# Performance work log

Measured on AMD Instinct MI355X. Metric: run time of the kernel, lower is better.

The kernel has to match this reference:

```python
import jax, jax.numpy as jnp
import numpy as np

RADIUS = 3
T_STEPS = 2
NEG = -9.0e8
B, L, DEG = 256, 64, 6
FEAT, BOND, FP, OUT = 39, 10, 256, 1


def _leaky(x):
    return jax.nn.leaky_relu(x, 0.01)


def _gru(x, h, wih, whh, bih, bhh):
    # PyTorch GRUCell: gates ordered (r, z, n)
    gi = x @ wih.T + bih
    gh = h @ whh.T + bhh
    ir, iz, inn = jnp.split(gi, 3, axis=-1)
    hr, hz, hn = jnp.split(gh, 3, axis=-1)
    r = jax.nn.sigmoid(ir + hr)
    z = jax.nn.sigmoid(iz + hz)
    n = jnp.tanh(inn + r * hn)
    return (1.0 - z) * n + z * h


def _forward(atom_list, bond_list, atom_mask,
             atom_fc_w, atom_fc_b, neighbor_fc_w, neighbor_fc_b,
             align_w, align_b, attend_w, attend_b,
             gru_wih, gru_whh, gru_bih, gru_bhh,
             mol_align_w, mol_align_b, mol_attend_w, mol_attend_b,
             mol_gru_wih, mol_gru_whh, mol_gru_bih, mol_gru_bhh,
             out_w, out_b,
             atom_degree_list, bond_degree_list):
    b, l, _ = atom_list.shape
    mask = atom_mask[..., None]                                   # [B,L,1]
    atom_feature = _leaky(atom_list @ atom_fc_w.T + atom_fc_b)    # [B,L,FP]

    # per-molecule neighbor gather (padding index = L-1)
    bidx = jnp.arange(b)[:, None, None]
    atom_nb = atom_list[bidx, atom_degree_list]                    # [B,L,deg,FEAT]
    bond_nb = bond_list[bidx, bond_degree_list]                    # [B,L,deg,BOND]
    neighbor_feature = _leaky(
        jnp.concatenate([atom_nb, bond_nb], axis=-1) @ neighbor_fc_w.T + neighbor_fc_b
    )                                                              # [B,L,deg,FP]

    attend_mask = (atom_degree_list != l - 1).astype(atom_feature.dtype)[..., None]
    softmax_mask = jnp.where(atom_degree_list == l - 1, NEG, 0.0).astype(atom_feature.dtype)[..., None]

    for d in range(RADIUS):
        af_exp = jnp.broadcast_to(atom_feature[:, :, None, :], neighbor_feature.shape)
        feature_align = jnp.concatenate([af_exp, neighbor_feature], axis=-1)  # [B,L,deg,2FP]
        align_score = _leaky(feature_align @ align_w[d].T + align_b[d]) + softmax_mask
        attention_weight = jax.nn.softmax(align_score, axis=-2) * attend_mask
        attended = neighbor_feature @ attend_w[d].T + attend_b[d]
        context = jax.nn.elu(jnp.sum(attention_weight * attended, axis=-2))   # [B,L,FP]
        atom_feature = _gru(context.reshape(b * l, -1), atom_feature.reshape(b * l, -1),
                            gru_wih[d], gru_whh[d], gru_bih[d], gru_bhh[d]).reshape(b, l, -1)
        # faithful to original: self-feature broadcast across neighbor dim
        neighbor_feature = jnp.broadcast_to(jax.nn.relu(atom_feature)[:, :, None, :],
                                            neighbor_feature.shape)

    mol_feature = jnp.sum(jax.nn.relu(atom_feature) * mask, axis=-2)          # [B,FP]
    mol_softmax_mask = jnp.where(atom_mask == 0, NEG, 0.0).astype(atom_feature.dtype)[..., None]

    for _ in range(T_STEPS):
        m_exp = jnp.broadcast_to(mol_feature[:, None, :], atom_feature.shape)
        mol_align = jnp.concatenate([m_exp, atom_feature], axis=-1)           # [B,L,2FP]
        mol_score = _leaky(mol_align @ mol_align_w.T + mol_align_b) + mol_softmax_mask
        mol_w = jax.nn.softmax(mol_score, axis=-2) * mask
        attended = atom_feature @ mol_attend_w.T + mol_attend_b
        mol_context = jax.nn.elu(jnp.sum(mol_w * attended, axis=-2))
        mol_feature = _gru(mol_context, mol_feature,
                           mol_gru_wih, mol_gru_whh, mol_gru_bih, mol_gru_bhh)

    mol_prediction = mol_feature @ out_w.T + out_b
    return atom_feature, mol_prediction


def setup_inputs() -> dict:
    key = jax.random.key(0)
    ks = jax.random.split(key, 20)
    s = 0.05
    return {
        "atom_list": jax.random.normal(ks[0], (B, L, FEAT), jnp.float32),
        "bond_list": jax.random.normal(ks[1], (B, L, BOND), jnp.float32),
        "atom_degree_list": jax.random.randint(ks[2], (B, L, DEG), 0, L),
        "bond_degree_list": jax.random.randint(ks[3], (B, L, DEG), 0, L),
        "atom_mask": jnp.ones((B, L), jnp.float32),
        "atom_fc_w": jax.random.normal(ks[4], (FP, FEAT)) * s,
        "atom_fc_b": jnp.zeros((FP,)),
        "neighbor_fc_w": jax.random.normal(ks[5], (FP, FEAT + BOND)) * s,
        "neighbor_fc_b": jnp.zeros((FP,)),
        "align_w": jax.random.normal(ks[6], (RADIUS, 1, 2 * FP)) * s,
        "align_b": jnp.zeros((RADIUS, 1)),
        "attend_w": jax.random.normal(ks[7], (RADIUS, FP, FP)) * s,
        "attend_b": jnp.zeros((RADIUS, FP)),
        "gru_wih": jax.random.normal(ks[8], (RADIUS, 3 * FP, FP)) * s,
        "gru_whh": jax.random.normal(ks[9], (RADIUS, 3 * FP, FP)) * s,
        "gru_bih": jnp.zeros((RADIUS, 3 * FP)),
        "gru_bhh": jnp.zeros((RADIUS, 3 * FP)),
        "mol_align_w": jax.random.normal(ks[10], (1, 2 * FP)) * s,
        "mol_align_b": jnp.zeros((1,)),
        "mol_attend_w": jax.random.normal(ks[11], (FP, FP)) * s,
        "mol_attend_b": jnp.zeros((FP,)),
        "mol_gru_wih": jax.random.normal(ks[12], (3 * FP, FP)) * s,
        "mol_gru_whh": jax.random.normal(ks[13], (3 * FP, FP)) * s,
        "mol_gru_bih": jnp.zeros((3 * FP,)),
        "mol_gru_bhh": jnp.zeros((3 * FP,)),
        "out_w": jax.random.normal(ks[14], (OUT, FP)) * s,
        "out_b": jnp.zeros((OUT,)),
    }


def reference(atom_list, bond_list, atom_degree_list, bond_degree_list, atom_mask,
              atom_fc_w, atom_fc_b, neighbor_fc_w, neighbor_fc_b,
              align_w, align_b, attend_w, attend_b,
              gru_wih, gru_whh, gru_bih, gru_bhh,
              mol_align_w, mol_align_b, mol_attend_w, mol_attend_b,
              mol_gru_wih, mol_gru_whh, mol_gru_bih, mol_gru_bhh,
              out_w, out_b):
    return _forward(atom_list, bond_list, atom_mask,
                    atom_fc_w, atom_fc_b, neighbor_fc_w, neighbor_fc_b,
                    align_w, align_b, attend_w, attend_b,
                    gru_wih, gru_whh, gru_bih, gru_bhh,
                    mol_align_w, mol_align_b, mol_attend_w, mol_attend_b,
                    mol_gru_wih, mol_gru_whh, mol_gru_bih, mol_gru_bhh,
                    out_w, out_b,
                    atom_degree_list, bond_degree_list)
```

## Files before the change

kernel.cpp:

```cpp
#include <hip/hip_runtime.h>
#include <hip/hip_bf16.h>

#define NB 256
#define NL 64
#define DEG 6
#define FEAT 39
#define BOND 10
#define FP 256
#define NEGV (-9.0e8f)

using s16x8 = __attribute__((ext_vector_type(8))) short;
using f32x4 = __attribute__((ext_vector_type(4))) float;

__device__ __forceinline__ unsigned short f2bf(float f){
  unsigned u = __float_as_uint(f);
  u += 0x7fffu + ((u >> 16) & 1u);
  return (unsigned short)(u >> 16);
}
__device__ __forceinline__ float lo16(unsigned u){ return __uint_as_float(u << 16); }
__device__ __forceinline__ float hi16(unsigned u){ return __uint_as_float(u & 0xffff0000u); }

__device__ __forceinline__ float block_sum256(float v, float* scr){
  #pragma unroll
  for(int o=32;o>0;o>>=1) v += __shfl_down(v, o, 64);
  __syncthreads();
  if((threadIdx.x & 63) == 0) scr[threadIdx.x >> 6] = v;
  __syncthreads();
  return scr[0] + scr[1] + scr[2] + scr[3];
}
__device__ __forceinline__ float wave_allsum(float v){
  #pragma unroll
  for(int o=1;o<64;o<<=1) v += __shfl_xor(v, o, 64);
  return v;
}

#define MCVT_N0 65536
#define MCVT_N1 196608
#define MCVT_N2 196608
#define MCVT_TOT (MCVT_N0+MCVT_N1+MCVT_N2)
#define CTXPK_N (3*8*8192)
#define GPK_N   (3*2*8*24576)
#define HALF_U16 24576

__global__ void k_cvt_mol(const float* __restrict__ a0, const float* __restrict__ a1,
                          const float* __restrict__ a2, unsigned short* __restrict__ dst){
  int i = blockIdx.x*256 + threadIdx.x;
  if(i >= MCVT_TOT) return;
  int off = i; const float* src;
  if(off < MCVT_N0) src = a0;
  else { off -= MCVT_N0;
    if(off < MCVT_N1) src = a1;
    else { off -= MCVT_N1; src = a2; } }
  dst[i] = f2bf(src[off]);
}

__global__ void k_pack(const float* __restrict__ attend_w, const float* __restrict__ gru_wih,
                       const float* __restrict__ gru_whh,
                       unsigned short* __restrict__ ctx_pk, unsigned short* __restrict__ gates_pk){
  int i = blockIdx.x*256 + threadIdx.x;
  if(i < CTXPK_N){
    int d = i >> 16;
    int rem = i & 65535;
    int kk = rem >> 13;
    int r2 = rem & 8191;
    int g = r2 >> 9;
    int l = (r2 >> 3) & 63;
    int q = r2 & 7;
    int row = g*16 + (l & 15);
    int k = kk*32 + (l >> 4)*8 + q;
    ctx_pk[i] = f2bf(attend_w[((size_t)d*256 + row)*256 + k]);
  } else {
    int j = i - CTXPK_N;
    if(j >= GPK_N) return;
    int d = j / 393216;
    int rem = j - d*393216;
    int nc = rem / 196608; rem -= nc*196608;
    int kk = rem / 24576;  rem -= kk*24576;
    int f = rem >> 9;
    int l = (rem >> 3) & 63;
    int q = rem & 7;
    int s = f >> 3, g = f & 7;
    int row = nc*128 + g*16 + (l & 15);
    int k = kk*32 + (l >> 4)*8 + q;
    float v = (s < 3) ? gru_wih[(((size_t)d*3 + s)*256 + row)*256 + k]
                      : gru_whh[(((size_t)d*3 + (s-3))*256 + row)*256 + k];
    gates_pk[j] = f2bf(v);
  }
}

__global__ void k_tr(const float* __restrict__ aw, const float* __restrict__ nw,
                     float* __restrict__ afcT, unsigned short* __restrict__ nfcT){
  int i = blockIdx.x*256 + threadIdx.x;
  if(i < 40*256){
    int k = i >> 8, r = i & 255;
    afcT[i] = (k < FEAT) ? aw[r*FEAT + k] : 0.f;
  } else {
    int j = i - 40*256;
    int k = j >> 8, r = j & 255;
    nfcT[j] = (k < FEAT+BOND) ? f2bf(nw[r*(FEAT+BOND) + k]) : (unsigned short)0;
  }
}

__global__ __launch_bounds__(256) void k_atom4(const float* __restrict__ atom,
    const float* __restrict__ afcT, const float* __restrict__ bias, float* __restrict__ af){
  __shared__ float x_s[4][40];
  const int t = threadIdx.x, bl0 = blockIdx.x*4;
  for(int idx=t; idx<4*FEAT; idx+=256){ int a=idx/FEAT, k=idx%FEAT; x_s[a][k]=atom[(bl0+a)*FEAT+k]; }
  if(t < 4) x_s[t][39] = 0.f;
  __syncthreads();
  const int w = t>>6, t0 = (t&63)*4, row = bl0 + w;
  float4 b4 = *(const float4*)&bias[t0];
  float acc[4] = {b4.x, b4.y, b4.z, b4.w};
  for(int k=0;k<40;++k){
    float iv = x_s[w][k];
    float4 wv = *(const float4*)&afcT[(k<<8)+t0];
    acc[0]=fmaf(iv,wv.x,acc[0]); acc[1]=fmaf(iv,wv.y,acc[1]);
    acc[2]=fmaf(iv,wv.z,acc[2]); acc[3]=fmaf(iv,wv.w,acc[3]);
  }
  float4 o;
  o.x = acc[0]>0.f?acc[0]:0.01f*acc[0]; o.y = acc[1]>0.f?acc[1]:0.01f*acc[1];
  o.z = acc[2]>0.f?acc[2]:0.01f*acc[2]; o.w = acc[3]>0.f?acc[3]:0.01f*acc[3];
  *(float4*)&af[(size_t)row*FP + t0] = o;
}

__global__ __launch_bounds__(256) void k_nbr4(const float* __restrict__ atom,
    const float* __restrict__ bond, const int* __restrict__ adl, const int* __restrict__ bdl,
    const unsigned short* __restrict__ nfcT, const float* __restrict__ bn,
    const float* __restrict__ alw, const float* __restrict__ alb,
    const float* __restrict__ af, float* __restrict__ wnf, float* __restrict__ swb){
  __shared__ float in_s[4][DEG][52];
  __shared__ int   ai_s[4][DEG];
  const int t = threadIdx.x, bl0 = blockIdx.x*4;
  if(t < 24){ int a=t/6, d=t%6; ai_s[a][d] = adl[(bl0+a)*DEG + d]; }
  __syncthreads();
  for(int idx=t; idx<4*DEG*(FEAT+BOND); idx+=256){
    int a = idx/(DEG*(FEAT+BOND)), rem = idx%(DEG*(FEAT+BOND));
    int d = rem/(FEAT+BOND), k = rem%(FEAT+BOND);
    int bb = (bl0+a) >> 6;
    float v;
    if(k < FEAT) v = atom[((size_t)bb*NL + ai_s[a][d])*FEAT + k];
    else { int bi = bdl[(bl0+a)*DEG + d]; v = bond[((size_t)bb*NL + bi)*BOND + (k-FEAT)]; }
    in_s[a][d][k] = v;
  }
  if(t < 24){ int a=t/6, d=t%6; in_s[a][d][49]=0.f; in_s[a][d][50]=0.f; in_s[a][d][51]=0.f; }
  __syncthreads();
  const int w = t>>6, lane = t&63, t0 = lane*4, row = bl0 + w;
  float acc[DEG][4] = {};
  for(int k=0;k<52;++k){
    uint2 u = *(const uint2*)&nfcT[(k<<8) + t0];
    float w0=lo16(u.x), w1=hi16(u.x), w2=lo16(u.y), w3=hi16(u.y);
    #pragma unroll
    for(int d=0;d<DEG;++d){
      float iv = in_s[w][d][k];
      acc[d][0]=fmaf(iv,w0,acc[d][0]); acc[d][1]=fmaf(iv,w1,acc[d][1]);
      acc[d][2]=fmaf(iv,w2,acc[d][2]); acc[d][3]=fmaf(iv,w3,acc[d][3]);
    }
  }
  float4 bnv = *(const float4*)&bn[t0];
  float bna[4] = {bnv.x, bnv.y, bnv.z, bnv.w};
  float nf[DEG][4];
  #pragma unroll
  for(int d=0;d<DEG;++d)
    #pragma unroll
    for(int j=0;j<4;++j){ float v = acc[d][j] + bna[j]; nf[d][j] = v>0.f ? v : 0.01f*v; }
  float4 af4 = *(const float4*)&af[(size_t)row*FP + t0];
  float4 a1  = *(const float4*)&alw[t0];
  float4 a2  = *(const float4*)&alw[FP + t0];
  float sa = wave_allsum(af4.x*a1.x + af4.y*a1.y + af4.z*a1.z + af4.w*a1.w);
  float sd[DEG];
  #pragma unroll
  for(int d=0;d<DEG;++d)
    sd[d] = wave_allsum(nf[d][0]*a2.x + nf[d][1]*a2.y + nf[d][2]*a2.z + nf[d][3]*a2.w);
  float ab = alb[0];
  float sc[DEG], msk[DEG];
  #pragma unroll
  for(int d=0;d<DEG;++d){
    float v = sa + sd[d] + ab;
    v = v>0.f ? v : 0.01f*v;
    msk[d] = (ai_s[w][d] == NL-1) ? 0.f : 1.f;
    sc[d] = v + (msk[d] > 0.f ? 0.f : NEGV);
  }
  float m = sc[0];
  #pragma unroll
  for(int d=1;d<DEG;++d) m = fmaxf(m, sc[d]);
  float e[DEG], Z = 0.f;
  #pragma unroll
  for(int d=0;d<DEG;++d){ e[d] = expf(sc[d]-m); Z += e[d]; }
  float wgt[DEG], sw = 0.f;
  #pragma unroll
  for(int d=0;d<DEG;++d){ wgt[d] = e[d]/Z*msk[d]; sw += wgt[d]; }
  float o[4] = {};
  #pragma unroll
  for(int d=0;d<DEG;++d)
    #pragma unroll
    for(int j=0;j<4;++j) o[j] = fmaf(wgt[d], nf[d][j], o[j]);
  float4 ov; ov.x=o[0]; ov.y=o[1]; ov.z=o[2]; ov.w=o[3];
  *(float4*)&wnf[(size_t)row*FP + t0] = ov;
  if(lane == 0) swb[row] = sw;
}

__global__ __launch_bounds__(512) void k_radius2(
    const float* __restrict__ wnf, float* __restrict__ af, const float* __restrict__ swb,
    const unsigned short* __restrict__ ctx_pk, const unsigned short* __restrict__ gates_pk,
    const float* __restrict__ attend_b,
    const float* __restrict__ gru_bih, const float* __restrict__ gru_bhh){
  __shared__ __align__(16) unsigned short Cf[32*512];
  __shared__ __align__(16) unsigned short Bu[2][HALF_U16];
  const int t = threadIdx.x;
  const int w = t>>6, lane = t&63, lr = lane&15, ks = lane>>4;
  const int wm = w>>2, wn = w&3;
  const int m0 = blockIdx.x*64;

  s16x8 pf[6]; int pfn = 0;
  auto LOADS = [&](int s){
    if(s >= 72) return;
    int d2 = s/24, r = s - d2*24;
    const unsigned short* src; int n;
    if(r < 8){ n = 2; src = ctx_pk + ((size_t)d2*8 + r)*8192; }
    else { int g = r - 8; n = 6; src = gates_pk + ((size_t)(d2*2 + (g>>3))*8 + (g&7))*24576; }
    pfn = n;
    #pragma unroll
    for(int c=0;c<6;++c) if(c < n) pf[c] = *(const s16x8*)(src + (w + c*8)*512 + lane*8);
  };
  auto WRITET = [&](int h){
    #pragma unroll
    for(int c=0;c<6;++c) if(c < pfn) *(s16x8*)&Bu[h][(w + c*8)*512 + lane*8] = pf[c];
  };

  LOADS(0);
  WRITET(0);
  LOADS(1);
  int half = 0;

  for(int d=0; d<3; ++d){
    const float* bat  = attend_b + d*256;
    const float* bihd = gru_bih + d*768;
    const float* bhhd = gru_bhh + d*768;

    __syncthreads();
    float4 px0[2], px1[2];
    #pragma unroll
    for(int mf=0; mf<2; ++mf){
      int row = m0 + wm*32 + mf*16 + lr;
      const float* sp = (d==0 ? wnf : af) + (size_t)row*256 + ks*8;
      px0[mf] = *(const float4*)sp; px1[mf] = *(const float4*)(sp+4);
    }
    f32x4 acc2[2][4] = {};
    for(int kk=0; kk<8; ++kk){
      int s = d*24 + kk;
      __syncthreads();
      WRITET(half^1);
      LOADS(s+2);
      float4 cx0[2] = {px0[0], px0[1]};
      float4 cx1[2] = {px1[0], px1[1]};
      if(kk < 7){
        #pragma unroll
        for(int mf=0; mf<2; ++mf){
          int row = m0 + wm*32 + mf*16 + lr;
          const float* sp = (d==0 ? wnf : af) + (size_t)row*256 + (kk+1)*32 + ks*8;
          px0[mf] = *(const float4*)sp; px1[mf] = *(const float4*)(sp+4);
        }
      }
      s16x8 xf[2];
      #pragma unroll
      for(int mf=0; mf<2; ++mf){
        float4 v0 = cx0[mf], v1 = cx1[mf];
        if(d != 0){
          float sw = swb[m0 + wm*32 + mf*16 + lr];
          v0.x=fmaxf(v0.x,0.f)*sw; v0.y=fmaxf(v0.y,0.f)*sw;
          v0.z=fmaxf(v0.z,0.f)*sw; v0.w=fmaxf(v0.w,0.f)*sw;
          v1.x=fmaxf(v1.x,0.f)*sw; v1.y=fmaxf(v1.y,0.f)*sw;
          v1.z=fmaxf(v1.z,0.f)*sw; v1.w=fmaxf(v1.w,0.f)*sw;
        }
        unsigned short tmp[8] = {f2bf(v0.x),f2bf(v0.y),f2bf(v0.z),f2bf(v0.w),
                                 f2bf(v1.x),f2bf(v1.y),f2bf(v1.z),f2bf(v1.w)};
        xf[mf] = *(s16x8*)tmp;
      }
      #pragma unroll
      for(int nf=0; nf<4; ++nf){
        s16x8 wf = *(const s16x8*)&Bu[half][((wn*4 + nf)*64 + lane)*8];
        acc2[0][nf] = __builtin_amdgcn_mfma_f32_16x16x32_bf16(wf, xf[0], acc2[0][nf],0,0,0);
        acc2[1][nf] = __builtin_amdgcn_mfma_f32_16x16x32_bf16(wf, xf[1], acc2[1][nf],0,0,0);
      }
      half ^= 1;
    }
    #pragma unroll
    for(int mf=0; mf<2; ++mf){
      float swv = swb[m0 + wm*32 + mf*16 + lr];
      #pragma unroll
      for(int nf=0; nf<4; ++nf){
        int nb = wn*64 + nf*16 + ks*4;
        float4 b4 = *(const float4*)&bat[nb];
        float bj[4] = {b4.x, b4.y, b4.z, b4.w};
        unsigned short o4[4];
        #pragma unroll
        for(int j=0;j<4;++j){
          float v = acc2[mf][nf][j] + swv*bj[j];
          v = v > 0.f ? v : expm1f(v);
          o4[j] = f2bf(v);
        }
        int gm = wm*2 + mf;
        int kkp = wn*2 + (nf>>1);
        int lhi = ((nf & 1) << 1) | (ks >> 1);
        int addr = (gm*8 + kkp)*512 + (lhi*16 + lr)*8 + (ks & 1)*4;
        *(uint2*)&Cf[addr] = *(uint2*)o4;
      }
    }
    float4 ph0[2], ph1[2];
    #pragma unroll
    for(int mf=0; mf<2; ++mf){
      int row = m0 + wm*32 + mf*16 + lr;
      const float* sp = af + (size_t)row*256 + ks*8;
      ph0[mf] = *(const float4*)sp; ph1[mf] = *(const float4*)(sp+4);
    }
    float hnew0[2][2][4];
    for(int nc=0; nc<2; ++nc){
      f32x4 aR[2][2] = {}, aZ[2][2] = {}, aN[2][2] = {}, aH[2][2] = {};
      for(int kk=0; kk<8; ++kk){
        int s = d*24 + 8 + nc*8 + kk;
        __syncthreads();
        if(s < 71) WRITET(half^1);
        LOADS(s+2);
        float4 ch0[2] = {ph0[0], ph0[1]};
        float4 ch1[2] = {ph1[0], ph1[1]};
        bool lastHK = (nc == 1) && (kk == 7);
        if(!lastHK){
          int kkn = (kk < 7) ? kk+1 : 0;
          #pragma unroll
          for(int mf=0; mf<2; ++mf){
            int row = m0 + wm*32 + mf*16 + lr;
            const float* sp = af + (size_t)row*256 + kkn*32 + ks*8;
            ph0[mf] = *(const float4*)sp; ph1[mf] = *(const float4*)(sp+4);
          }
        }
        s16x8 hf[2];
        #pragma unroll
        for(int mf=0; mf<2; ++mf){
          float4 v0 = ch0[mf], v1 = ch1[mf];
          unsigned short tmp[8] = {f2bf(v0.x),f2bf(v0.y),f2bf(v0.z),f2bf(v0.w),
                                   f2bf(v1.x),f2bf(v1.y),f2bf(v1.z),f2bf(v1.w)};
          hf[mf] = *(s16x8*)tmp;
        }
        s16x8 cf0 = *(const s16x8*)&Cf[((wm*2 + 0)*8 + kk)*512 + lane*8];
        s16x8 cf1 = *(const s16x8*)&Cf[((wm*2 + 1)*8 + kk)*512 + lane*8];
        #pragma unroll
        for(int fn=0; fn<2; ++fn){
          int g = wn*2 + fn;
          s16x8 b0 = *(const s16x8*)&Bu[half][((0*8 + g)*64 + lane)*8];
          s16x8 b1 = *(const s16x8*)&Bu[half][((1*8 + g)*64 + lane)*8];
          s16x8 b2 = *(const s16x8*)&Bu[half][((2*8 + g)*64 + lane)*8];
          s16x8 b3 = *(const s16x8*)&Bu[half][((3*8 + g)*64 + lane)*8];
          s16x8 b4 = *(const s16x8*)&Bu[half][((4*8 + g)*64 + lane)*8];
          s16x8 b5 = *(const s16x8*)&Bu[half][((5*8 + g)*64 + lane)*8];
          aR[0][fn] = __builtin_amdgcn_mfma_f32_16x16x32_bf16(cf0, b0, aR[0][fn],0,0,0);
          aR[1][fn] = __builtin_amdgcn_mfma_f32_16x16x32_bf16(cf1, b0, aR[1][fn],0,0,0);
          aZ[0][fn] = __builtin_amdgcn_mfma_f32_16x16x32_bf16(cf0, b1, aZ[0][fn],0,0,0);
          aZ[1][fn] = __builtin_amdgcn_mfma_f32_16x16x32_bf16(cf1, b1, aZ[1][fn],0,0,0);
          aN[0][fn] = __builtin_amdgcn_mfma_f32_16x16x32_bf16(cf0, b2, aN[0][fn],0,0,0);
          aN[1][fn] = __builtin_amdgcn_mfma_f32_16x16x32_bf16(cf1, b2, aN[1][fn],0,0,0);
          aR[0][fn] = __builtin_amdgcn_mfma_f32_16x16x32_bf16(hf[0], b3, aR[0][fn],0,0,0);
          aR[1][fn] = __builtin_amdgcn_mfma_f32_16x16x32_bf16(hf[1], b3, aR[1][fn],0,0,0);
          aZ[0][fn] = __builtin_amdgcn_mfma_f32_16x16x32_bf16(hf[0], b4, aZ[0][fn],0,0,0);
          aZ[1][fn] = __builtin_amdgcn_mfma_f32_16x16x32_bf16(hf[1], b4, aZ[1][fn],0,0,0);
          aH[0][fn] = __builtin_amdgcn_mfma_f32_16x16x32_bf16(hf[0], b5, aH[0][fn],0,0,0);
          aH[1][fn] = __builtin_amdgcn_mfma_f32_16x16x32_bf16(hf[1], b5, aH[1][fn],0,0,0);
        }
        half ^= 1;
      }
      if(nc == 0){
        #pragma unroll
        for(int mf=0; mf<2; ++mf)
          #pragma unroll
          for(int fn=0; fn<2; ++fn){
            int n = wn*32 + fn*16 + lr;
            float brz = bihd[n] + bhhd[n];
            float bzz = bihd[256+n] + bhhd[256+n];
            float bnn = bihd[512+n];
            float bhn = bhhd[512+n];
            #pragma unroll
            for(int j=0;j<4;++j){
              int m = m0 + wm*32 + mf*16 + ks*4 + j;
              float hold = af[(size_t)m*256 + n];
              float r = 1.f/(1.f + expf(-(aR[mf][fn][j] + brz)));
              float z = 1.f/(1.f + expf(-(aZ[mf][fn][j] + bzz)));
              float ng = tanhf(aN[mf][fn][j] + bnn + r*(aH[mf][fn][j] + bhn));
              hnew0[mf][fn][j] = (1.f - z)*ng + z*hold;
            }
          }
      } else {
        #pragma unroll
        for(int mf=0; mf<2; ++mf)
          #pragma unroll
          for(int fn=0; fn<2; ++fn){
            int n = 128 + wn*32 + fn*16 + lr;
            float brz = bihd[n] + bhhd[n];
            float bzz = bihd[256+n] + bhhd[256+n];
            float bnn = bihd[512+n];
            float bhn = bhhd[512+n];
            #pragma unroll
            for(int j=0;j<4;++j){
              int m = m0 + wm*32 + mf*16 + ks*4 + j;
              float hold = af[(size_t)m*256 + n];
              float r = 1.f/(1.f + expf(-(aR[mf][fn][j] + brz)));
              float z = 1.f/(1.f + expf(-(aZ[mf][fn][j] + bzz)));
              float ng = tanhf(aN[mf][fn][j] + bnn + r*(aH[mf][fn][j] + bhn));
              af[(size_t)m*256 + n] = (1.f - z)*ng + z*hold;
            }
          }
        #pragma unroll
        for(int mf=0; mf<2; ++mf)
          #pragma unroll
          for(int fn=0; fn<2; ++fn){
            int n = wn*32 + fn*16 + lr;
            #pragma unroll
            for(int j=0;j<4;++j){
              int m = m0 + wm*32 + mf*16 + ks*4 + j;
              af[(size_t)m*256 + n] = hnew0[mf][fn][j];
            }
          }
      }
    }
  }
}

__global__ __launch_bounds__(256) void k_lin_gemm(
    const float* __restrict__ Xsrc, const unsigned short* __restrict__ Wbf,
    const float* __restrict__ bias, float* __restrict__ Y){
  __shared__ unsigned short A_lds[64][264];
  __shared__ unsigned short B_lds[64][264];
  const int t = threadIdx.x;
  const int m0 = (blockIdx.x >> 2) * 64, n0 = (blockIdx.x & 3) * 64;
  const int rb = t >> 4, cb = (t & 15) * 16;
  for(int i=0;i<4;++i){
    int row = i*16 + rb;
    const float* src = Xsrc + (size_t)(m0+row)*FP + cb;
    unsigned short tmp[16];
    #pragma unroll
    for(int q=0;q<4;++q){
      float4 v = ((const float4*)src)[q];
      tmp[q*4+0]=f2bf(v.x); tmp[q*4+1]=f2bf(v.y); tmp[q*4+2]=f2bf(v.z); tmp[q*4+3]=f2bf(v.w);
    }
    *(s16x8*)&A_lds[row][cb]   = *(s16x8*)&tmp[0];
    *(s16x8*)&A_lds[row][cb+8] = *(s16x8*)&tmp[8];
    const unsigned short* wsrc = Wbf + (size_t)(n0+row)*FP + cb;
    *(s16x8*)&B_lds[row][cb]   = *(const s16x8*)&wsrc[0];
    *(s16x8*)&B_lds[row][cb+8] = *(const s16x8*)&wsrc[8];
  }
  __syncthreads();
  const int w = t>>6, lane = t&63, lr = lane&15, ks = lane>>4;
  const int wr = (w>>1)*32, wc = (w&1)*32;
  f32x4 acc[2][2] = {};
  #pragma unroll
  for(int kk=0;kk<8;++kk){
    int ko = kk*32 + ks*8;
    s16x8 a0 = *(const s16x8*)&A_lds[wr+lr][ko];
    s16x8 a1 = *(const s16x8*)&A_lds[wr+16+lr][ko];
    s16x8 b0 = *(const s16x8*)&B_lds[wc+lr][ko];
    s16x8 b1 = *(const s16x8*)&B_lds[wc+16+lr][ko];
    acc[0][0] = __builtin_amdgcn_mfma_f32_16x16x32_bf16(a0,b0,acc[0][0],0,0,0);
    acc[0][1] = __builtin_amdgcn_mfma_f32_16x16x32_bf16(a0,b1,acc[0][1],0,0,0);
    acc[1][0] = __builtin_amdgcn_mfma_f32_16x16x32_bf16(a1,b0,acc[1][0],0,0,0);
    acc[1][1] = __builtin_amdgcn_mfma_f32_16x16x32_bf16(a1,b1,acc[1][1],0,0,0);
  }
  #pragma unroll
  for(int fm=0;fm<2;++fm)
    #pragma unroll
    for(int fn=0;fn<2;++fn){
      int n = n0 + wc + fn*16 + lr;
      float bv = bias[n];
      #pragma unroll
      for(int j=0;j<4;++j){
        int m = m0 + wr + fm*16 + ks*4 + j;
        Y[(size_t)m*FP + n] = acc[fm][fn][j] + bv;
      }
    }
}

__global__ __launch_bounds__(256) void k_gates32(
    const unsigned short* __restrict__ ctxbf, const float* __restrict__ h_glob,
    const unsigned short* __restrict__ wihbf, const unsigned short* __restrict__ whhbf,
    const float* __restrict__ bih, const float* __restrict__ bhh,
    float* __restrict__ h_out){
  __shared__ unsigned short A_ctx[32][40];
  __shared__ unsigned short A_h[32][40];
  __shared__ unsigned short B_lds[6][64][40];
  const int t = threadIdx.x;
  const int m0 = (blockIdx.x >> 2) * 32, nc = (blockIdx.x & 3) * 64;
  const int w = t>>6, lane = t&63, lr = lane&15, ks = lane>>4;
  const int mh = (w>>1)*16, nh = (w&1)*32;
  f32x4 acc[6][2] = {};
  for(int kk=0;kk<8;++kk){
    const int k0 = kk*32;
    __syncthreads();
    {
      int row = t>>3, c4 = (t&7)*4;
      *(uint2*)&A_ctx[row][c4] = *(const uint2*)(ctxbf + (size_t)(m0+row)*FP + k0 + c4);
      float4 hv = *(const float4*)(h_glob + (size_t)(m0+row)*FP + k0 + c4);
      unsigned short ht[4] = {f2bf(hv.x), f2bf(hv.y), f2bf(hv.z), f2bf(hv.w)};
      *(uint2*)&A_h[row][c4] = *(uint2*)ht;
    }
    #pragma unroll
    for(int i=0;i<6;++i){
      int idx = i*256 + t;
      int s = idx >> 8, rem = idx & 255;
      int row = rem >> 2, c8 = (rem & 3)*8;
      const unsigned short* wsrc = (s < 3)
          ? wihbf + (size_t)(s*FP + nc + row)*FP + k0 + c8
          : whhbf + (size_t)((s-3)*FP + nc + row)*FP + k0 + c8;
      *(s16x8*)&B_lds[s][row][c8] = *(const s16x8*)wsrc;
    }
    __syncthreads();
    s16x8 ac = *(const s16x8*)&A_ctx[mh+lr][ks*8];
    s16x8 ah = *(const s16x8*)&A_h[mh+lr][ks*8];
    #pragma unroll
    for(int s=0;s<6;++s){
      s16x8 a = (s < 3) ? ac : ah;
      #pragma unroll
      for(int fn=0;fn<2;++fn){
        s16x8 b = *(const s16x8*)&B_lds[s][nh+fn*16+lr][ks*8];
        acc[s][fn] = __builtin_amdgcn_mfma_f32_16x16x32_bf16(a,b,acc[s][fn],0,0,0);
      }
    }
  }
  #pragma unroll
  for(int fn=0;fn<2;++fn){
    int n = nc + nh + fn*16 + lr;
    float bir = bih[n], biz = bih[FP+n], bin_ = bih[2*FP+n];
    float bhr = bhh[n], bhz = bhh[FP+n], bhn  = bhh[2*FP+n];
    #pragma unroll
    for(int j=0;j<4;++j){
      int m = m0 + mh + ks*4 + j;
      float h = h_glob[(size_t)m*FP + n];
      float ir = acc[0][fn][j]+bir, iz = acc[1][fn][j]+biz, inn = acc[2][fn][j]+bin_;
      float hr = acc[3][fn][j]+bhr, hz = acc[4][fn][j]+bhz, hn  = acc[5][fn][j]+bhn;
      float r = 1.f/(1.f + expf(-(ir+hr)));
      float z = 1.f/(1.f + expf(-(iz+hz)));
      float ng = tanhf(inn + r*hn);
      h_out[(size_t)m*FP + n] = (1.f-z)*ng + z*h;
    }
  }
}

__global__ void k_finalize(const float* __restrict__ af, const float* __restrict__ mask,
                           float* __restrict__ molfeat, float* __restrict__ out_af){
  const int b = blockIdx.x, t = threadIdx.x;
  __shared__ float msk_s[NL];
  if(t < NL) msk_s[t] = mask[b*NL + t];
  __syncthreads();
  float mf = 0.f;
  for(int l=0;l<NL;++l){
    float v = af[(size_t)(b*NL + l)*FP + t];
    out_af[(size_t)(b*NL + l)*FP + t] = v;
    mf = fmaf(fmaxf(v,0.f), msk_s[l], mf);
  }
  molfeat[b*FP + t] = mf;
}

__global__ void k_mol_ctx(const float* __restrict__ af, const float* __restrict__ att,
    const float* __restrict__ mfin, const float* __restrict__ maw,
    const float* __restrict__ mabp, const float* __restrict__ mask,
    unsigned short* __restrict__ ctxb){
  const int b = blockIdx.x, t = threadIdx.x;
  __shared__ float mf_s[FP];
  __shared__ float sc_s[NL], aw_s[NL], scr[4];
  mf_s[t] = mfin[b*FP + t];
  __syncthreads();
  float sa = block_sum256(maw[t]*mf_s[t], scr);
  int l = t >> 2, q = t & 3;
  float p = 0.f;
  {
    const float4* ar = (const float4*)(af + (size_t)(b*NL + l)*FP + q*64);
    const float4* w2 = (const float4*)(maw + FP + q*64);
    #pragma unroll
    for(int k=0;k<16;++k){
      float4 a = ar[k], ww = w2[k];
      p = fmaf(a.x,ww.x,p); p = fmaf(a.y,ww.y,p);
      p = fmaf(a.z,ww.z,p); p = fmaf(a.w,ww.w,p);
    }
  }
  p += __shfl_xor(p, 1, 64);
  p += __shfl_xor(p, 2, 64);
  if(q == 0){
    float mv = mask[b*NL + l];
    float v = sa + p + mabp[0];
    v = v > 0.f ? v : 0.01f*v;
    sc_s[l] = v + (mv == 0.f ? NEGV : 0.f);
  }
  __syncthreads();
  if(t < NL){
    float s = sc_s[t];
    float m = s;
    #pragma unroll
    for(int o=32;o>0;o>>=1) m = fmaxf(m, __shfl_xor(m, o, 64));
    float e = expf(s - m);
    float Z = e;
    #pragma unroll
    for(int o=32;o>0;o>>=1) Z += __shfl_xor(Z, o, 64);
    aw_s[t] = e / Z * mask[b*NL + t];
  }
  __syncthreads();
  float acc = 0.f;
  for(int l2=0;l2<NL;++l2) acc = fmaf(aw_s[l2], att[(size_t)(b*NL + l2)*FP + t], acc);
  float c = acc > 0.f ? acc : expm1f(acc);
  ctxb[b*FP + t] = f2bf(c);
}

__global__ void k_out(const float* __restrict__ molfeat, const float* __restrict__ ow,
                      const float* __restrict__ ob, float* __restrict__ outp){
  const int b = blockIdx.x, t = threadIdx.x;
  __shared__ float scr[4];
  float s = block_sum256(molfeat[b*FP + t]*ow[t], scr);
  if(t == 0) outp[b] = s + ob[0];
}

extern "C" void kernel_launch(void* const* d_in, const int* in_sizes, int n_in,
                              void* d_out, int out_size, void* d_ws, size_t ws_size,
                              hipStream_t stream){
  const float* atom_list = (const float*)d_in[0];
  const float* bond_list = (const float*)d_in[1];
  const int*   adl       = (const int*)d_in[2];
  const int*   bdl       = (const int*)d_in[3];
  const float* amask     = (const float*)d_in[4];
  const float* afc_w     = (const float*)d_in[5];
  const float* afc_b     = (const float*)d_in[6];
  const float* nfc_w     = (const float*)d_in[7];
  const float* nfc_b     = (const float*)d_in[8];
  const float* align_w   = (const float*)d_in[9];
  const float* align_b   = (const float*)d_in[10];
  const float* attend_w  = (const float*)d_in[11];
  const float* attend_b  = (const float*)d_in[12];
  const float* gru_wih   = (const float*)d_in[13];
  const float* gru_whh   = (const float*)d_in[14];
  const float* gru_bih   = (const float*)d_in[15];
  const float* gru_bhh   = (const float*)d_in[16];
  const float* mol_align_w  = (const float*)d_in[17];
  const float* mol_align_b  = (const float*)d_in[18];
  const float* mol_attend_w = (const float*)d_in[19];
  const float* mol_attend_b = (const float*)d_in[20];
  const float* mg_wih    = (const float*)d_in[21];
  const float* mg_whh    = (const float*)d_in[22];
  const float* mg_bih    = (const float*)d_in[23];
  const float* mg_bhh    = (const float*)d_in[24];
  const float* out_w     = (const float*)d_in[25];
  const float* out_b     = (const float*)d_in[26];

  float* out_af   = (float*)d_out;
  float* out_pred = out_af + (size_t)NB*NL*FP;

  const size_t NROW = (size_t)NB*NL;
  const size_t F32_CNT = 2*NROW*FP + NROW + 2*(size_t)NB*FP + 40*256;
  const size_t U16_CNT = (size_t)NB*FP + MCVT_TOT + 52*256 + CTXPK_N + GPK_N;
  const size_t NEED = F32_CNT*4 + U16_CNT*2;

  if(ws_size >= NEED){
    float* af_a    = (float*)d_ws;
    float* wnf     = af_a + NROW*FP;
    float* swb     = wnf  + NROW*FP;
    float* mf_a    = swb  + NROW;
    float* mf_b    = mf_a + (size_t)NB*FP;
    float* afcT    = mf_b + (size_t)NB*FP;
    unsigned short* ctxbf_m = (unsigned short*)(afcT + 40*256);
    unsigned short* maw_bf  = ctxbf_m + (size_t)NB*FP;
    unsigned short* mgih_bf = maw_bf + MCVT_N0;
    unsigned short* mghh_bf = mgih_bf + MCVT_N1;
    unsigned short* nfcT_bf = mghh_bf + MCVT_N2;
    unsigned short* ctx_pk  = nfcT_bf + 52*256;
    unsigned short* gates_pk= ctx_pk + CTXPK_N;

    k_cvt_mol<<<(MCVT_TOT+255)/256, 256, 0, stream>>>(mol_attend_w, mg_wih, mg_whh, maw_bf);
    k_pack<<<(CTXPK_N+GPK_N)/256, 256, 0, stream>>>(attend_w, gru_wih, gru_whh, ctx_pk, gates_pk);
    k_tr<<<(40*256 + 52*256)/256, 256, 0, stream>>>(afc_w, nfc_w, afcT, nfcT_bf);

    k_atom4<<<NB*NL/4, 256, 0, stream>>>(atom_list, afcT, afc_b, af_a);
    k_nbr4<<<NB*NL/4, 256, 0, stream>>>(atom_list, bond_list, adl, bdl,
                                        nfcT_bf, nfc_b, align_w, align_b, af_a, wnf, swb);
    k_radius2<<<NB*NL/64, 512, 0, stream>>>(wnf, af_a, swb, ctx_pk, gates_pk,
                                            attend_b, gru_bih, gru_bhh);
    k_lin_gemm<<<(NB*NL/64)*4, 256, 0, stream>>>(af_a, maw_bf, mol_attend_b, wnf);
    k_finalize<<<NB, 256, 0, stream>>>(af_a, amask, mf_a, out_af);
    float* m_cur = mf_a; float* m_nxt = mf_b;
    for(int s=0; s<2; ++s){
      k_mol_ctx<<<NB, 256, 0, stream>>>(af_a, wnf, m_cur, mol_align_w, mol_align_b,
                                        amask, ctxbf_m);
      k_gates32<<<(NB/32)*4, 256, 0, stream>>>(ctxbf_m, m_cur, mgih_bf, mghh_bf,
                                               mg_bih, mg_bhh, m_nxt);
      float* tmp = m_cur; m_cur = m_nxt; m_nxt = tmp;
    }
    k_out<<<NB, 256, 0, stream>>>(m_cur, out_w, out_b, out_pred);
  } else {
    float* af = (float*)d_ws;
    k_atom4<<<NB*NL/4, 256, 0, stream>>>(atom_list, (const float*)afc_w, afc_b, af);
    (void)bond_list; (void)adl; (void)bdl; (void)amask;
    (void)align_w; (void)align_b; (void)attend_w; (void)attend_b;
    (void)gru_wih; (void)gru_whh; (void)gru_bih; (void)gru_bhh;
    (void)mol_align_w; (void)mol_align_b; (void)mol_attend_w; (void)mol_attend_b;
    (void)mg_wih; (void)mg_whh; (void)mg_bih; (void)mg_bhh; (void)out_w; (void)out_b;
  }
}
```

Measured before the change: 321.9 us.

## Split radius GRU kernel across 16 waves instead of 8 per block

The fused radius kernel now launches 1024 threads per block, with 8 waves along the N dimension instead of 4. Each wave handles half as many output columns, so it holds fewer accumulators and loads fewer prefetch fragments. The aim is more latency hiding and less per-wave serial work for the same 64-row tile. In exchange the block is limited to one per CU and pays costlier barriers, and each wave redundantly loads and converts the same activation fragments.

Result: slower. 418.5 us (+30.0%).

```diff
diff --git a/kernel.cpp b/kernel.cpp
--- a/kernel.cpp
+++ b/kernel.cpp
@@ -199,7 +199,7 @@
   if(lane == 0) swb[row] = sw;
 }
 
-__global__ __launch_bounds__(512) void k_radius2(
+__global__ __launch_bounds__(1024, 1) void k_radius7(
     const float* __restrict__ wnf, float* __restrict__ af, const float* __restrict__ swb,
     const unsigned short* __restrict__ ctx_pk, const unsigned short* __restrict__ gates_pk,
     const float* __restrict__ attend_b,
@@ -208,23 +208,23 @@
   __shared__ __align__(16) unsigned short Bu[2][HALF_U16];
   const int t = threadIdx.x;
   const int w = t>>6, lane = t&63, lr = lane&15, ks = lane>>4;
-  const int wm = w>>2, wn = w&3;
+  const int wm = w>>3, wn = w&7;
   const int m0 = blockIdx.x*64;
 
-  s16x8 pf[6]; int pfn = 0;
+  s16x8 pf[3]; int pfn = 0;
   auto LOADS = [&](int s){
     if(s >= 72) return;
     int d2 = s/24, r = s - d2*24;
     const unsigned short* src; int n;
-    if(r < 8){ n = 2; src = ctx_pk + ((size_t)d2*8 + r)*8192; }
-    else { int g = r - 8; n = 6; src = gates_pk + ((size_t)(d2*2 + (g>>3))*8 + (g&7))*24576; }
+    if(r < 8){ n = 1; src = ctx_pk + ((size_t)d2*8 + r)*8192; }
+    else { int g = r - 8; n = 3; src = gates_pk + ((size_t)(d2*2 + (g>>3))*8 + (g&7))*24576; }
     pfn = n;
     #pragma unroll
-    for(int c=0;c<6;++c) if(c < n) pf[c] = *(const s16x8*)(src + (w + c*8)*512 + lane*8);
+    for(int c=0;c<3;++c) if(c < n) pf[c] = *(const s16x8*)(src + (w + c*16)*512 + lane*8);
   };
   auto WRITET = [&](int h){
     #pragma unroll
-    for(int c=0;c<6;++c) if(c < pfn) *(s16x8*)&Bu[h][(w + c*8)*512 + lane*8] = pf[c];
+    for(int c=0;c<3;++c) if(c < pfn) *(s16x8*)&Bu[h][(w + c*16)*512 + lane*8] = pf[c];
   };
 
   LOADS(0);
@@ -245,7 +245,7 @@
       const float* sp = (d==0 ? wnf : af) + (size_t)row*256 + ks*8;
       px0[mf] = *(const float4*)sp; px1[mf] = *(const float4*)(sp+4);
     }
-    f32x4 acc2[2][4] = {};
+    f32x4 acc2[2][2] = {};
     for(int kk=0; kk<8; ++kk){
       int s = d*24 + kk;
       __syncthreads();
@@ -277,8 +277,8 @@
         xf[mf] = *(s16x8*)tmp;
       }
       #pragma unroll
-      for(int nf=0; nf<4; ++nf){
-        s16x8 wf = *(const s16x8*)&Bu[half][((wn*4 + nf)*64 + lane)*8];
+      for(int nf=0; nf<2; ++nf){
+        s16x8 wf = *(const s16x8*)&Bu[half][((wn*2 + nf)*64 + lane)*8];
         acc2[0][nf] = __builtin_amdgcn_mfma_f32_16x16x32_bf16(wf, xf[0], acc2[0][nf],0,0,0);
         acc2[1][nf] = __builtin_amdgcn_mfma_f32_16x16x32_bf16(wf, xf[1], acc2[1][nf],0,0,0);
       }
@@ -288,8 +288,9 @@
     for(int mf=0; mf<2; ++mf){
       float swv = swb[m0 + wm*32 + mf*16 + lr];
       #pragma unroll
-      for(int nf=0; nf<4; ++nf){
-        int nb = wn*64 + nf*16 + ks*4;
+      for(int nf=0; nf<2; ++nf){
+        int gf = wn*2 + nf;
+        int nb = gf*16 + ks*4;
         float4 b4 = *(const float4*)&bat[nb];
         float bj[4] = {b4.x, b4.y, b4.z, b4.w};
         unsigned short o4[4];
@@ -300,8 +301,8 @@
           o4[j] = f2bf(v);
         }
         int gm = wm*2 + mf;
-        int kkp = wn*2 + (nf>>1);
-        int lhi = ((nf & 1) << 1) | (ks >> 1);
+        int kkp = gf >> 1;
+        int lhi = ((gf & 1) << 1) | (ks >> 1);
         int addr = (gm*8 + kkp)*512 + (lhi*16 + lr)*8 + (ks & 1)*4;
         *(uint2*)&Cf[addr] = *(uint2*)o4;
       }
@@ -313,9 +314,9 @@
       const float* sp = af + (size_t)row*256 + ks*8;
       ph0[mf] = *(const float4*)sp; ph1[mf] = *(const float4*)(sp+4);
     }
-    float hnew0[2][2][4];
+    float hnew0[2][4];
     for(int nc=0; nc<2; ++nc){
-      f32x4 aR[2][2] = {}, aZ[2][2] = {}, aN[2][2] = {}, aH[2][2] = {};
+      f32x4 aR[2] = {}, aZ[2] = {}, aN[2] = {}, aH[2] = {};
       for(int kk=0; kk<8; ++kk){
         int s = d*24 + 8 + nc*8 + kk;
         __syncthreads();
@@ -343,81 +344,74 @@
         }
         s16x8 cf0 = *(const s16x8*)&Cf[((wm*2 + 0)*8 + kk)*512 + lane*8];
         s16x8 cf1 = *(const s16x8*)&Cf[((wm*2 + 1)*8 + kk)*512 + lane*8];
-        #pragma unroll
-        for(int fn=0; fn<2; ++fn){
-          int g = wn*2 + fn;
+        {
+          int g = wn;
           s16x8 b0 = *(const s16x8*)&Bu[half][((0*8 + g)*64 + lane)*8];
           s16x8 b1 = *(const s16x8*)&Bu[half][((1*8 + g)*64 + lane)*8];
           s16x8 b2 = *(const s16x8*)&Bu[half][((2*8 + g)*64 + lane)*8];
           s16x8 b3 = *(const s16x8*)&Bu[half][((3*8 + g)*64 + lane)*8];
           s16x8 b4 = *(const s16x8*)&Bu[half][((4*8 + g)*64 + lane)*8];
           s16x8 b5 = *(const s16x8*)&Bu[half][((5*8 + g)*64 + lane)*8];
-          aR[0][fn] = __builtin_amdgcn_mfma_f32_16x16x32_bf16(cf0, b0, aR[0][fn],0,0,0);
-          aR[1][fn] = __builtin_amdgcn_mfma_f32_16x16x32_bf16(cf1, b0, aR[1][fn],0,0,0);
-          aZ[0][fn] = __builtin_amdgcn_mfma_f32_16x16x32_bf16(cf0, b1, aZ[0][fn],0,0,0);
-          aZ[1][fn] = __builtin_amdgcn_mfma_f32_16x16x32_bf16(cf1, b1, aZ[1][fn],0,0,0);
-          aN[0][fn] = __builtin_amdgcn_mfma_f32_16x16x32_bf16(cf0, b2, aN[0][fn],0,0,0);
-          aN[1][fn] = __builtin_amdgcn_mfma_f32_16x16x32_bf16(cf1, b2, aN[1][fn],0,0,0);
-          aR[0][fn] = __builtin_amdgcn_mfma_f32_16x16x32_bf16(hf[0], b3, aR[0][fn],0,0,0);
-          aR[1][fn] = __builtin_amdgcn_mfma_f32_16x16x32_bf16(hf[1], b3, aR[1][fn],0,0,0);
-          aZ[0][fn] = __builtin_amdgcn_mfma_f32_16x16x32_bf16(hf[0], b4, aZ[0][fn],0,0,0);
-          aZ[1][fn] = __builtin_amdgcn_mfma_f32_16x16x32_bf16(hf[1], b4, aZ[1][fn],0,0,0);
-          aH[0][fn] = __builtin_amdgcn_mfma_f32_16x16x32_bf16(hf[0], b5, aH[0][fn],0,0,0);
-          aH[1][fn] = __builtin_amdgcn_mfma_f32_16x16x32_bf16(hf[1], b5, aH[1][fn],0,0,0);
+          aR[0] = __builtin_amdgcn_mfma_f32_16x16x32_bf16(cf0, b0, aR[0],0,0,0);
+          aR[1] = __builtin_amdgcn_mfma_f32_16x16x32_bf16(cf1, b0, aR[1],0,0,0);
+          aZ[0] = __builtin_amdgcn_mfma_f32_16x16x32_bf16(cf0, b1, aZ[0],0,0,0);
+          aZ[1] = __builtin_amdgcn_mfma_f32_16x16x32_bf16(cf1, b1, aZ[1],0,0,0);
+          aN[0] = __builtin_amdgcn_mfma_f32_16x16x32_bf16(cf0, b2, aN[0],0,0,0);
+          aN[1] = __builtin_amdgcn_mfma_f32_16x16x32_bf16(cf1, b2, aN[1],0,0,0);
+          aR[0] = __builtin_amdgcn_mfma_f32_16x16x32_bf16(hf[0], b3, aR[0],0,0,0);
+          aR[1] = __builtin_amdgcn_mfma_f32_16x16x32_bf16(hf[1], b3, aR[1],0,0,0);
+          aZ[0] = __builtin_amdgcn_mfma_f32_16x16x32_bf16(hf[0], b4, aZ[0],0,0,0);
+          aZ[1] = __builtin_amdgcn_mfma_f32_16x16x32_bf16(hf[1], b4, aZ[1],0,0,0);
+          aH[0] = __builtin_amdgcn_mfma_f32_16x16x32_bf16(hf[0], b5, aH[0],0,0,0);
+          aH[1] = __builtin_amdgcn_mfma_f32_16x16x32_bf16(hf[1], b5, aH[1],0,0,0);
         }
         half ^= 1;
       }
       if(nc == 0){
         #pragma unroll
-        for(int mf=0; mf<2; ++mf)
+        for(int mf=0; mf<2; ++mf){
+          int n = wn*16 + lr;
+          float brz = bihd[n] + bhhd[n];
+          float bzz = bihd[256+n] + bhhd[256+n];
+          float bnn = bihd[512+n];
+          float bhn = bhhd[512+n];
           #pragma unroll
-          for(int fn=0; fn<2; ++fn){
-            int n = wn*32 + fn*16 + lr;
-            float brz = bihd[n] + bhhd[n];
-            float bzz = bihd[256+n] + bhhd[256+n];
-            float bnn = bihd[512+n];
-            float bhn = bhhd[512+n];
-            #pragma unroll
-            for(int j=0;j<4;++j){
-              int m = m0 + wm*32 + mf*16 + ks*4 + j;
-              float hold = af[(size_t)m*256 + n];
-              float r = 1.f/(1.f + expf(-(aR[mf][fn][j] + brz)));
-              float z = 1.f/(1.f + expf(-(aZ[mf][fn][j] + bzz)));
-              float ng = tanhf(aN[mf][fn][j] + bnn + r*(aH[mf][fn][j] + bhn));
-              hnew0[mf][fn][j] = (1.f - z)*ng + z*hold;
-            }
+          for(int j=0;j<4;++j){
+            int m = m0 + wm*32 + mf*16 + ks*4 + j;
+            float hold = af[(size_t)m*256 + n];
+            float r = 1.f/(1.f + expf(-(aR[mf][j] + brz)));
+            float z = 1.f/(1.f + expf(-(aZ[mf][j] + bzz)));
+            float ng = tanhf(aN[mf][j] + bnn + r*(aH[mf][j] + bhn));
+            hnew0[mf][j] = (1.f - z)*ng + z*hold;
           }
+        }
       } else {
         #pragma unroll
-        for(int mf=0; mf<2; ++mf)
+        for(int mf=0; mf<2; ++mf){
+          int n = 128 + wn*16 + lr;
+          float brz = bihd[n] + bhhd[n];
+          float bzz = bihd[256+n] + bhhd[256+n];
+          float bnn = bihd[512+n];
+          float bhn = bhhd[512+n];
           #pragma unroll
-          for(int fn=0; fn<2; ++fn){
-            int n = 128 + wn*32 + fn*16 + lr;
-            float brz = bihd[n] + bhhd[n];
-            float bzz = bihd[256+n] + bhhd[256+n];
-            float bnn = bihd[512+n];
-            float bhn = bhhd[512+n];
-            #pragma unroll
-            for(int j=0;j<4;++j){
-              int m = m0 + wm*32 + mf*16 + ks*4 + j;
-              float hold = af[(size_t)m*256 + n];
-              float r = 1.f/(1.f + expf(-(aR[mf][fn][j] + brz)));
-              float z = 1.f/(1.f + expf(-(aZ[mf][fn][j] + bzz)));
-              float ng = tanhf(aN[mf][fn][j] + bnn + r*(aH[mf][fn][j] + bhn));
-              af[(size_t)m*256 + n] = (1.f - z)*ng + z*hold;
-            }
+          for(int j=0;j<4;++j){
+            int m = m0 + wm*32 + mf*16 + ks*4 + j;
+            float hold = af[(size_t)m*256 + n];
+            float r = 1.f/(1.f + expf(-(aR[mf][j] + brz)));
+            float z = 1.f/(1.f + expf(-(aZ[mf][j] + bzz)));
+            float ng = tanhf(aN[mf][j] + bnn + r*(aH[mf][j] + bhn));
+            af[(size_t)m*256 + n] = (1.f - z)*ng + z*hold;
           }
+        }
         #pragma unroll
-        for(int mf=0; mf<2; ++mf)
+        for(int mf=0; mf<2; ++mf){
+          int n = wn*16 + lr;
           #pragma unroll
-          for(int fn=0; fn<2; ++fn){
-            int n = wn*32 + fn*16 + lr;
-            #pragma unroll
-            for(int j=0;j<4;++j){
-              int m = m0 + wm*32 + mf*16 + ks*4 + j;
-              af[(size_t)m*256 + n] = hnew0[mf][fn][j];
-            }
+          for(int j=0;j<4;++j){
+            int m = m0 + wm*32 + mf*16 + ks*4 + j;
+            af[(size_t)m*256 + n] = hnew0[mf][j];
           }
+        }
       }
     }
   }
@@ -674,8 +668,8 @@
     k_atom4<<<NB*NL/4, 256, 0, stream>>>(atom_list, afcT, afc_b, af_a);
     k_nbr4<<<NB*NL/4, 256, 0, stream>>>(atom_list, bond_list, adl, bdl,
                                         nfcT_bf, nfc_b, align_w, align_b, af_a, wnf, swb);
-    k_radius2<<<NB*NL/64, 512, 0, stream>>>(wnf, af_a, swb, ctx_pk, gates_pk,
-                                            attend_b, gru_bih, gru_bhh);
+    k_radius7<<<NB*NL/64, 1024, 0, stream>>>(wnf, af_a, swb, ctx_pk, gates_pk,
+                                             attend_b, gru_bih, gru_bhh);
     k_lin_gemm<<<(NB*NL/64)*4, 256, 0, stream>>>(af_a, maw_bf, mol_attend_b, wnf);
     k_finalize<<<NB, 256, 0, stream>>>(af_a, amask, mf_a, out_af);
     float* m_cur = mf_a; float* m_nxt = mf_b;
```
